# Kernel optimization log

Measured on AMD Instinct MI355X. Metric: run time of the kernel, lower is better.

The kernel has to match this reference:

```python
import jax, jax.numpy as jnp
import numpy as np

B, S, D, H = 2, 2048, 1024, 16
DK = D // H
THETA = 10000.0


def apply_rope(x, pos, theta):
    # x: [B, H, S, DK], pos: [S]
    dk = x.shape[-1]
    inv_freq = 1.0 / (theta ** (jnp.arange(0, dk, 2, dtype=jnp.float32) / dk))  # [DK/2]
    ang = pos.astype(jnp.float32)[:, None] * inv_freq[None, :]  # [S, DK/2]
    cos, sin = jnp.cos(ang), jnp.sin(ang)
    x1 = x[..., 0::2]  # even dims
    x2 = x[..., 1::2]  # odd dims
    r1 = x1 * cos - x2 * sin
    r2 = x1 * sin + x2 * cos
    # re-interleave pairs back into last dim
    return jnp.stack([r1, r2], axis=-1).reshape(x.shape)


def setup_inputs() -> dict:
    key = jax.random.key(0)
    k1, k2, k3 = jax.random.split(key, 3)
    in_features = jax.random.normal(k1, (B, S, D), dtype=jnp.float32)
    token_positions = jnp.arange(S, dtype=jnp.int32)
    Wqkv = jax.random.normal(k2, (D, 3 * D), dtype=jnp.float32) * 0.02
    Wo = jax.random.normal(k3, (D, D), dtype=jnp.float32) * 0.02
    return {"in_features": in_features, "token_positions": token_positions,
            "Wqkv": Wqkv, "Wo": Wo}


def reference(in_features, token_positions, Wqkv, Wo):
    x = in_features
    qkv = x @ Wqkv  # [B, S, 3D]
    Q, K, V = jnp.split(qkv, 3, axis=-1)

    def to_heads(t):  # [B, S, D] -> [B, H, S, DK]
        return t.reshape(B, S, H, DK).transpose(0, 2, 1, 3)

    Q, K, V = to_heads(Q), to_heads(K), to_heads(V)
    Q = apply_rope(Q, token_positions, THETA)
    K = apply_rope(K, token_positions, THETA)

    scale = 1.0 / jnp.sqrt(jnp.float32(DK))
    scores = jnp.einsum("bhqd,bhkd->bhqk", Q, K) * scale  # [B, H, S, S]
    causal = jnp.tril(jnp.ones((S, S), dtype=bool))
    scores = jnp.where(causal, scores, jnp.finfo(scores.dtype).min)
    attn = jax.nn.softmax(scores, axis=-1)
    out = jnp.einsum("bhqk,bhkd->bhqd", attn, V)  # [B, H, S, DK]
    out = out.transpose(0, 2, 1, 3).reshape(B, S, D)
    return out @ Wo
```

## Files before the change

### kernel.cpp

```cpp
#include <hip/hip_runtime.h>
#include <hip/hip_bf16.h>
#include <math.h>

typedef unsigned short u16;
typedef unsigned int u32;
typedef __attribute__((ext_vector_type(4))) float f32x4;
typedef __attribute__((ext_vector_type(8))) short bf16x8;

#define B_ 2
#define S_ 2048
#define D_ 1024
#define H_ 16
#define DK_ 64

__device__ __forceinline__ float exp2_fast(float x) {
    return __builtin_amdgcn_exp2f(x);
}

__device__ __forceinline__ u16 f2bf(float x) {
    union { __hip_bfloat16 h; u16 u; } v;
    v.h = __float2bfloat16(x);
    return v.u;
}

__device__ __forceinline__ u32 cvt_pk_bf16(float a, float b) {
    u32 r;
    asm("v_cvt_pk_bf16_f32 %0, %1, %2" : "=v"(r) : "v"(a), "v"(b));
    return r;
}

__device__ __forceinline__ void gload_lds16(const u16* g, u16* l) {
    __builtin_amdgcn_global_load_lds(
        (const __attribute__((address_space(1))) unsigned int*)g,
        (__attribute__((address_space(3))) unsigned int*)l, 16, 0, 0);
}

__global__ __launch_bounds__(256) void cast_bf16_kernel(
    const float* __restrict__ in, u16* __restrict__ outp, int n)
{
    const int i = (blockIdx.x * 256 + threadIdx.x) * 8;
    if (i >= n) return;
    float4 a = *(const float4*)(in + i);
    float4 b = *(const float4*)(in + i + 4);
    u32 p0 = (u32)f2bf(a.x) | ((u32)f2bf(a.y) << 16);
    u32 p1 = (u32)f2bf(a.z) | ((u32)f2bf(a.w) << 16);
    u32 p2 = (u32)f2bf(b.x) | ((u32)f2bf(b.y) << 16);
    u32 p3 = (u32)f2bf(b.z) | ((u32)f2bf(b.w) << 16);
    *(uint4*)(outp + i) = make_uint4(p0, p1, p2, p3);
}

__global__ __launch_bounds__(256) void transpose_cast(
    const float* __restrict__ W, u16* __restrict__ WT, int N)
{
    __shared__ float tile[64][65];
    const int k0 = blockIdx.x * 64, n0 = blockIdx.y * 64;
    const int t = threadIdx.x;
    const int r = t >> 4, c4 = (t & 15) * 4;
#pragma unroll
    for (int p = 0; p < 4; ++p) {
        float4 v = *(const float4*)&W[(size_t)(k0 + r + p * 16) * N + n0 + c4];
        tile[r + p * 16][c4 + 0] = v.x;
        tile[r + p * 16][c4 + 1] = v.y;
        tile[r + p * 16][c4 + 2] = v.z;
        tile[r + p * 16][c4 + 3] = v.w;
    }
    __syncthreads();
    const int nl = t >> 2, kc = (t & 3) * 16;
    u16 buf[16];
#pragma unroll
    for (int j = 0; j < 16; ++j) buf[j] = f2bf(tile[kc + j][nl]);
    const size_t idx = (size_t)(n0 + nl) * 1024 + k0 + kc;
    u32 px[8];
#pragma unroll
    for (int j = 0; j < 8; ++j) px[j] = (u32)buf[2 * j] | ((u32)buf[2 * j + 1] << 16);
    *(uint4*)&WT[idx]     = make_uint4(px[0], px[1], px[2], px[3]);
    *(uint4*)&WT[idx + 8] = make_uint4(px[4], px[5], px[6], px[7]);
}

__global__ __launch_bounds__(256) void rope_table_kernel(
    const int* __restrict__ pos, float2* __restrict__ tab)
{
    const int i = blockIdx.x * 256 + threadIdx.x;
    const int s = i >> 5, j = i & 31;
    const float freq = __powf(10000.f, -(float)(2 * j) * (1.f / 64.f));
    const float ang = (float)pos[s] * freq;
    float sn, cs;
    sincosf(ang, &sn, &cs);
    tab[i] = make_float2(cs, sn);
}

__device__ __forceinline__ void gemm_mainloop_128x64(
    const u16* __restrict__ A, const u16* __restrict__ BT, int K,
    int m0, int n0, int tid, int l, int w,
    u16* lA, u16* lB, f32x4 acc[2][4])
{
    const int wr = w >> 1, wc = w & 1, lr = l & 15, lg = l >> 4;
    const int srow = tid >> 3;
    const int cg   = (tid & 7) ^ (srow & 7);
    const u16* gA = A + (size_t)(m0 + srow) * K + cg * 8;
    const u16* gB = BT + (size_t)(n0 + srow) * K + cg * 8;
    const int dst0 = tid * 8;

#define GSTAGE(k0, off)                                              \
    do {                                                             \
        gload_lds16(gA + (k0),          lA + (off) + dst0);          \
        gload_lds16(gA + (k0) + 64 * K, lA + (off) + 4096 + dst0);   \
        gload_lds16(gB + (k0),          lB + (off) + dst0);          \
        gload_lds16(gB + (k0) + 64 * K, lB + (off) + 4096 + dst0);   \
    } while (0)

    GSTAGE(0, 0);

    const int NT = K >> 6;
    for (int t = 0; t < NT; ++t) {
        const int coff = (t & 1) * 8192;
        if (t + 1 < NT) {
            GSTAGE((t + 1) * 64, coff ^ 8192);
            asm volatile("s_waitcnt vmcnt(4)" ::: "memory");
        } else {
            asm volatile("s_waitcnt vmcnt(0)" ::: "memory");
        }
        __builtin_amdgcn_s_barrier();
        __builtin_amdgcn_sched_barrier(0);

        bf16x8 a[2][2], b[4][2];
#pragma unroll
        for (int i = 0; i < 2; ++i) {
            const int row = wr * 32 + i * 16 + lr;
#pragma unroll
            for (int s = 0; s < 2; ++s)
                a[i][s] = *(const bf16x8*)(lA + coff + row * 64 + (((s * 4 + lg) ^ (row & 7)) * 8));
        }
#pragma unroll
        for (int j = 0; j < 4; ++j) {
            const int row = wc * 64 + j * 16 + lr;
#pragma unroll
            for (int s = 0; s < 2; ++s)
                b[j][s] = *(const bf16x8*)(lB + coff + row * 64 + (((s * 4 + lg) ^ (row & 7)) * 8));
        }
#pragma unroll
        for (int s = 0; s < 2; ++s)
#pragma unroll
            for (int i = 0; i < 2; ++i)
#pragma unroll
                for (int j = 0; j < 4; ++j)
                    acc[i][j] = __builtin_amdgcn_mfma_f32_16x16x32_bf16(a[i][s], b[j][s], acc[i][j], 0, 0, 0);

        asm volatile("s_waitcnt lgkmcnt(0)" ::: "memory");
        __builtin_amdgcn_s_barrier();
        __builtin_amdgcn_sched_barrier(0);
    }
#undef GSTAGE
}

__global__ __launch_bounds__(512, 4) void gemm_qkv_rope(
    const u16* __restrict__ A, const u16* __restrict__ BT,
    const float2* __restrict__ tab,
    u16* __restrict__ qo, u16* __restrict__ ko, u16* __restrict__ vto)
{
    __shared__ u16 lA[2 * 128 * 64];
    __shared__ u16 lB[2 * 128 * 64];
    const int tid = threadIdx.x, l = tid & 63, w = tid >> 6;
    const int m0 = blockIdx.x * 128, n0 = blockIdx.y * 128;

    f32x4 acc[2][4] = {};
    gemm_mainloop_128x64(A, BT, 1024, m0, n0, tid, l, w, lA, lB, acc);

    const int wr = w >> 1, wc = w & 1, lr = l & 15, lg = l >> 4;
    const int region = n0 >> 10;

    if (region < 2) {
        u16* dst = (region == 0) ? qo : ko;
        const float qscale = (region == 0) ? (0.125f * 1.44269504088896f) : 1.0f;
#pragma unroll
        for (int j = 0; j < 4; ++j) {
            const int nb = n0 + wc * 64 + j * 16;
            const int h = (nb >> 6) & 15;
            const int c = j * 16 + lr;
#pragma unroll
            for (int i = 0; i < 2; ++i) {
#pragma unroll
                for (int r = 0; r < 4; ++r) {
                    const int m = m0 + wr * 32 + i * 16 + lg * 4 + r;
                    const int bb = m >> 11, s = m & (S_ - 1);
                    const float2 cs = tab[s * 32 + (c >> 1)];
                    const float v = acc[i][j][r];
                    const float vp = __shfl_xor(v, 1);
                    float outv = ((lr & 1) == 0) ? (v * cs.x - vp * cs.y)
                                                 : (v * cs.x + vp * cs.y);
                    outv *= qscale;
                    dst[(((size_t)bb * H_ + h) * S_ + s) * DK_ + c] = f2bf(outv);
                }
            }
        }
    } else {
#pragma unroll
        for (int j = 0; j < 4; ++j) {
            const int nb = n0 + wc * 64 + j * 16;
            const int h = (nb >> 6) & 15;
            const int c = j * 16 + lr;
#pragma unroll
            for (int i = 0; i < 2; ++i) {
#pragma unroll
                for (int r = 0; r < 4; ++r) {
                    const int m = m0 + wr * 32 + i * 16 + lg * 4 + r;
                    const int bb = m >> 11, s = m & (S_ - 1);
                    vto[(((size_t)bb * H_ + h) * DK_ + c) * S_ + s] = f2bf(acc[i][j][r]);
                }
            }
        }
    }
}

__device__ __forceinline__ void stage_tile(
    const u16* __restrict__ Kbh, const u16* __restrict__ Vbh, int kt,
    u16* sKb, u16* sVb, int w, int sr0, int cg)
{
    gload_lds16(Kbh + ((size_t)kt * 64 + sr0) * DK_ + cg * 8,     sKb + w * 1024);
    gload_lds16(Kbh + ((size_t)kt * 64 + sr0 + 8) * DK_ + cg * 8, sKb + w * 1024 + 512);
    gload_lds16(Vbh + (size_t)sr0 * S_ + kt * 64 + cg * 8,        sVb + w * 1024);
    gload_lds16(Vbh + (size_t)(sr0 + 8) * S_ + kt * 64 + cg * 8,  sVb + w * 1024 + 512);
}

__device__ __forceinline__ void attn_stripe(
    int qt, int bh, int w, int l, int lr, int lg,
    const u16* __restrict__ Qg, const u16* __restrict__ Kg,
    const u16* __restrict__ VTg, u16* __restrict__ Og,
    u16 (*sK)[64 * 64], u16 (*sV)[64 * 64])
{
    const int q0 = qt * 64 + w * 16;
    const u16* Kbh = Kg + (size_t)bh * S_ * DK_;
    const u16* Vbh = VTg + (size_t)bh * DK_ * S_;

    const u16* Qp = Qg + ((size_t)bh * S_ + q0) * DK_;
    bf16x8 qa[2];
    qa[0] = *(const bf16x8*)(Qp + lr * DK_ + lg * 8);
    qa[1] = *(const bf16x8*)(Qp + lr * DK_ + 32 + lg * 8);

    const int sr0 = w * 16 + (l >> 3);
    const int cg  = (l & 7) ^ (sr0 & 7);

    f32x4 o[4] = {};
    float mi = -3.0e38f, li = 0.f;

    const int s0 = lr + 32 * (lg & 1);
    const int s1 = s0 + 16;
    const bool hi2 = (lg >= 2);

    stage_tile(Kbh, Vbh, 0, sK[0], sV[0], w, sr0, cg);
    asm volatile("s_waitcnt vmcnt(0)" ::: "memory");
    __syncthreads();

    for (int kt = 0; kt <= qt; ++kt) {
        const int cur = kt & 1;
        if (kt < qt)
            stage_tile(Kbh, Vbh, kt + 1, sK[cur ^ 1], sV[cur ^ 1], w, sr0, cg);

        f32x4 s4[4] = {};
        __builtin_amdgcn_s_setprio(1);
#pragma unroll
        for (int kf = 0; kf < 4; ++kf) {
            const int row = kf * 16 + lr;
#pragma unroll
            for (int ks = 0; ks < 2; ++ks) {
                bf16x8 kb = *(const bf16x8*)(&sK[cur][row * 64 + (((ks * 4 + lg) ^ (row & 7)) * 8)]);
                s4[kf] = __builtin_amdgcn_mfma_f32_16x16x32_bf16(kb, qa[ks], s4[kf], 0, 0, 0);
            }
        }
        __builtin_amdgcn_s_setprio(0);
        if (kt == qt) {
            const int qloc = w * 16 + lr;
#pragma unroll
            for (int kf = 0; kf < 4; ++kf)
#pragma unroll
                for (int r = 0; r < 4; ++r)
                    if (kf * 16 + lg * 4 + r > qloc) s4[kf][r] = -3.0e38f;
        }

        float mx = s4[0][0];
#pragma unroll
        for (int kf = 0; kf < 4; ++kf)
#pragma unroll
            for (int r = 0; r < 4; ++r) mx = fmaxf(mx, s4[kf][r]);
        mx = fmaxf(mx, __shfl_xor(mx, 16));
        mx = fmaxf(mx, __shfl_xor(mx, 32));
        if (mx > mi + 8.0f) {
            const float al = exp2_fast(mi - mx);
            mi = mx;
            li *= al;
#pragma unroll
            for (int jf = 0; jf < 4; ++jf)
#pragma unroll
                for (int r = 0; r < 4; ++r) o[jf][r] *= al;
        }
        float rs = 0.f;
#pragma unroll
        for (int kf = 0; kf < 4; ++kf)
#pragma unroll
            for (int r = 0; r < 4; ++r) {
                const float p = exp2_fast(s4[kf][r] - mi);
                s4[kf][r] = p;
                rs += p;
            }
        rs += __shfl_xor(rs, 16);
        rs += __shfl_xor(rs, 32);
        li += rs;

        u32 pk[4][2];
#pragma unroll
        for (int kf = 0; kf < 4; ++kf) {
            pk[kf][0] = cvt_pk_bf16(s4[kf][0], s4[kf][1]);
            pk[kf][1] = cvt_pk_bf16(s4[kf][2], s4[kf][3]);
        }
        union { u32 wd[4]; bf16x8 v; } pa[2];
#pragma unroll
        for (int ks = 0; ks < 2; ++ks) {
            const u32 lo0 = pk[2 * ks][0],     lo1 = pk[2 * ks][1];
            const u32 hi0 = pk[2 * ks + 1][0], hi1 = pk[2 * ks + 1][1];
            const u32 a0 = __shfl(lo0, s0), b0 = __shfl(hi0, s0);
            const u32 a1 = __shfl(lo1, s0), b1 = __shfl(hi1, s0);
            const u32 a2 = __shfl(lo0, s1), b2 = __shfl(hi0, s1);
            const u32 a3 = __shfl(lo1, s1), b3 = __shfl(hi1, s1);
            pa[ks].wd[0] = hi2 ? b0 : a0;
            pa[ks].wd[1] = hi2 ? b1 : a1;
            pa[ks].wd[2] = hi2 ? b2 : a2;
            pa[ks].wd[3] = hi2 ? b3 : a3;
        }

        __builtin_amdgcn_s_setprio(1);
#pragma unroll
        for (int ks = 0; ks < 2; ++ks) {
#pragma unroll
            for (int jf = 0; jf < 4; ++jf) {
                const int row = jf * 16 + lr;
                bf16x8 vb = *(const bf16x8*)(&sV[cur][row * 64 + (((ks * 4 + lg) ^ (row & 7)) * 8)]);
                o[jf] = __builtin_amdgcn_mfma_f32_16x16x32_bf16(vb, pa[ks].v, o[jf], 0, 0, 0);
            }
        }
        __builtin_amdgcn_s_setprio(0);

        asm volatile("s_waitcnt vmcnt(0)" ::: "memory");
        __syncthreads();
    }

    const float inv = 1.f / li;
    const int b = bh >> 4, h = bh & 15;
    const int srow = q0 + lr;
    u16* orow = Og + ((size_t)b * S_ + srow) * D_ + h * DK_;
#pragma unroll
    for (int jf = 0; jf < 4; ++jf) {
#pragma unroll
        for (int p = 0; p < 2; ++p) {
            const u32 wv = cvt_pk_bf16(o[jf][2 * p] * inv, o[jf][2 * p + 1] * inv);
            *(u32*)(orow + jf * 16 + lg * 4 + 2 * p) = wv;
        }
    }
}

__global__ __launch_bounds__(256) void attn_mfma(
    const u16* __restrict__ Qg, const u16* __restrict__ Kg,
    const u16* __restrict__ VTg, u16* __restrict__ Og)
{
    __shared__ u16 sK[2][64 * 64];
    __shared__ u16 sV[2][64 * 64];
    const int t = threadIdx.x, l = t & 63, w = t >> 6;
    const int lr = l & 15, lg = l >> 4;
    const int bh = blockIdx.x;
    const int qt = 31 - blockIdx.y;
    attn_stripe(qt, bh, w, l, lr, lg, Qg, Kg, VTg, Og, sK, sV);
}

__global__ __launch_bounds__(512, 4) void gemm_out(
    const u16* __restrict__ A, const u16* __restrict__ BT, float* __restrict__ C)
{
    __shared__ u16 lA[2 * 128 * 64];
    __shared__ u16 lB[2 * 128 * 64];
    const int tid = threadIdx.x, l = tid & 63, w = tid >> 6;
    const int m0 = blockIdx.x * 128, n0 = blockIdx.y * 128;

    f32x4 acc[2][4] = {};
    gemm_mainloop_128x64(A, BT, 1024, m0, n0, tid, l, w, lA, lB, acc);

    const int wr = w >> 1, wc = w & 1, lr = l & 15, lg = l >> 4;
#pragma unroll
    for (int j = 0; j < 4; ++j) {
        const int n = n0 + wc * 64 + j * 16 + lr;
#pragma unroll
        for (int i = 0; i < 2; ++i) {
#pragma unroll
            for (int r = 0; r < 4; ++r) {
                const int m = m0 + wr * 32 + i * 16 + lg * 4 + r;
                C[(size_t)m * D_ + n] = acc[i][j][r];
            }
        }
    }
}

extern "C" void kernel_launch(void* const* d_in, const int* in_sizes, int n_in,
                              void* d_out, int out_size, void* d_ws, size_t ws_size,
                              hipStream_t stream) {
    const float* X    = (const float*)d_in[0];
    const int*   pos  = (const int*)d_in[1];
    const float* Wqkv = (const float*)d_in[2];
    const float* Wo   = (const float*)d_in[3];
    float* out = (float*)d_out;

    char* ws = (char*)d_ws;
    u16*    Xb  = (u16*)(ws);
    u16*    WqT = (u16*)(ws + ((size_t)8  << 20));
    u16*    WoT = (u16*)(ws + ((size_t)14 << 20));
    float2* tab = (float2*)(ws + ((size_t)16 << 20));
    u16*    Qb  = (u16*)(ws + ((size_t)17 << 20));
    u16*    Kb  = (u16*)(ws + ((size_t)25 << 20));
    u16*    VTb = (u16*)(ws + ((size_t)33 << 20));
    u16*    AOb = (u16*)(ws + ((size_t)41 << 20));

    cast_bf16_kernel<<<2048, 256, 0, stream>>>(X, Xb, B_ * S_ * D_);
    transpose_cast<<<dim3(16, 48), 256, 0, stream>>>(Wqkv, WqT, 3 * D_);
    transpose_cast<<<dim3(16, 16), 256, 0, stream>>>(Wo, WoT, D_);
    rope_table_kernel<<<256, 256, 0, stream>>>(pos, tab);

    gemm_qkv_rope<<<dim3(32, 24), 512, 0, stream>>>(Xb, WqT, tab, Qb, Kb, VTb);
    attn_mfma<<<dim3(32, 32), 256, 0, stream>>>(Qb, Kb, VTb, AOb);
    gemm_out<<<dim3(32, 8), 512, 0, stream>>>(AOb, WoT, out);
}
```

Measured before the change: 119.9 us.

## Widen attention KV tile from 64 to 128 keys per iteration

The attention kernel now stages 128-key K/V tiles per loop iteration instead of 64, halving the number of iterations, barriers and softmax rescale steps. The LDS layout changes to 128-wide V rows with a 16-way XOR swizzle, and the causal mask now covers the diagonal 128-block using the query's position inside it. In exchange, LDS use doubles, register pressure rises with s4[8] and pa[4], and for odd query tiles half of the last key tile is computed and then masked, which is wasted work.

```diff
diff --git a/kernel.cpp b/kernel.cpp
--- a/kernel.cpp
+++ b/kernel.cpp
@@ -212,23 +212,21 @@
     }
 }
 
-__device__ __forceinline__ void stage_tile(
-    const u16* __restrict__ Kbh, const u16* __restrict__ Vbh, int kt,
-    u16* sKb, u16* sVb, int w, int sr0, int cg)
-{
-    gload_lds16(Kbh + ((size_t)kt * 64 + sr0) * DK_ + cg * 8,     sKb + w * 1024);
-    gload_lds16(Kbh + ((size_t)kt * 64 + sr0 + 8) * DK_ + cg * 8, sKb + w * 1024 + 512);
-    gload_lds16(Vbh + (size_t)sr0 * S_ + kt * 64 + cg * 8,        sVb + w * 1024);
-    gload_lds16(Vbh + (size_t)(sr0 + 8) * S_ + kt * 64 + cg * 8,  sVb + w * 1024 + 512);
-}
-
-__device__ __forceinline__ void attn_stripe(
-    int qt, int bh, int w, int l, int lr, int lg,
+__global__ __launch_bounds__(256) void attn_mfma(
     const u16* __restrict__ Qg, const u16* __restrict__ Kg,
-    const u16* __restrict__ VTg, u16* __restrict__ Og,
-    u16 (*sK)[64 * 64], u16 (*sV)[64 * 64])
-{
+    const u16* __restrict__ VTg, u16* __restrict__ Og)
+{
+    __shared__ u16 sK[2][128 * 64];
+    __shared__ u16 sV[2][64 * 128];
+    const int t = threadIdx.x, l = t & 63, w = t >> 6;
+    const int lr = l & 15, lg = l >> 4;
+    const int bh = blockIdx.x;
+    const int qt = 31 - blockIdx.y;
     const int q0 = qt * 64 + w * 16;
+    const int dt = qt >> 1;
+    const int NT = dt + 1;
+    const int qloc = (qt & 1) * 64 + w * 16 + lr;
+
     const u16* Kbh = Kg + (size_t)bh * S_ * DK_;
     const u16* Vbh = VTg + (size_t)bh * DK_ * S_;
 
@@ -237,8 +235,24 @@
     qa[0] = *(const bf16x8*)(Qp + lr * DK_ + lg * 8);
     qa[1] = *(const bf16x8*)(Qp + lr * DK_ + 32 + lg * 8);
 
-    const int sr0 = w * 16 + (l >> 3);
-    const int cg  = (l & 7) ^ (sr0 & 7);
+    const int kcg = (l & 7) ^ (l >> 3);
+
+#define STAGE(kt, b)                                                          \
+    do {                                                                      \
+        _Pragma("unroll")                                                     \
+        for (int i = 0; i < 4; ++i) {                                         \
+            const int kr = w * 32 + i * 8 + (l >> 3);                         \
+            gload_lds16(Kbh + ((size_t)(kt) * 128 + kr) * DK_ + kcg * 8,      \
+                        &sK[b][(w * 32 + i * 8) * 64]);                       \
+        }                                                                     \
+        _Pragma("unroll")                                                     \
+        for (int i = 0; i < 4; ++i) {                                         \
+            const int vr = w * 16 + i * 4 + (l >> 4);                         \
+            const int vc = (l & 15) ^ ((i * 4 + (l >> 4)) & 15);              \
+            gload_lds16(Vbh + (size_t)vr * S_ + (kt) * 128 + vc * 8,          \
+                        &sV[b][(w * 16 + i * 4) * 128]);                      \
+        }                                                                     \
+    } while (0)
 
     f32x4 o[4] = {};
     float mi = -3.0e38f, li = 0.f;
@@ -247,19 +261,18 @@
     const int s1 = s0 + 16;
     const bool hi2 = (lg >= 2);
 
-    stage_tile(Kbh, Vbh, 0, sK[0], sV[0], w, sr0, cg);
+    STAGE(0, 0);
     asm volatile("s_waitcnt vmcnt(0)" ::: "memory");
     __syncthreads();
 
-    for (int kt = 0; kt <= qt; ++kt) {
+    for (int kt = 0; kt < NT; ++kt) {
         const int cur = kt & 1;
-        if (kt < qt)
-            stage_tile(Kbh, Vbh, kt + 1, sK[cur ^ 1], sV[cur ^ 1], w, sr0, cg);
-
-        f32x4 s4[4] = {};
+        if (kt + 1 < NT) STAGE(kt + 1, cur ^ 1);
+
+        f32x4 s4[8] = {};
         __builtin_amdgcn_s_setprio(1);
 #pragma unroll
-        for (int kf = 0; kf < 4; ++kf) {
+        for (int kf = 0; kf < 8; ++kf) {
             const int row = kf * 16 + lr;
 #pragma unroll
             for (int ks = 0; ks < 2; ++ks) {
@@ -268,10 +281,9 @@
             }
         }
         __builtin_amdgcn_s_setprio(0);
-        if (kt == qt) {
-            const int qloc = w * 16 + lr;
-#pragma unroll
-            for (int kf = 0; kf < 4; ++kf)
+        if (kt == dt) {
+#pragma unroll
+            for (int kf = 0; kf < 8; ++kf)
 #pragma unroll
                 for (int r = 0; r < 4; ++r)
                     if (kf * 16 + lg * 4 + r > qloc) s4[kf][r] = -3.0e38f;
@@ -279,7 +291,7 @@
 
         float mx = s4[0][0];
 #pragma unroll
-        for (int kf = 0; kf < 4; ++kf)
+        for (int kf = 0; kf < 8; ++kf)
 #pragma unroll
             for (int r = 0; r < 4; ++r) mx = fmaxf(mx, s4[kf][r]);
         mx = fmaxf(mx, __shfl_xor(mx, 16));
@@ -295,7 +307,7 @@
         }
         float rs = 0.f;
 #pragma unroll
-        for (int kf = 0; kf < 4; ++kf)
+        for (int kf = 0; kf < 8; ++kf)
 #pragma unroll
             for (int r = 0; r < 4; ++r) {
                 const float p = exp2_fast(s4[kf][r] - mi);
@@ -306,15 +318,15 @@
         rs += __shfl_xor(rs, 32);
         li += rs;
 
-        u32 pk[4][2];
-#pragma unroll
-        for (int kf = 0; kf < 4; ++kf) {
+        u32 pk[8][2];
+#pragma unroll
+        for (int kf = 0; kf < 8; ++kf) {
             pk[kf][0] = cvt_pk_bf16(s4[kf][0], s4[kf][1]);
             pk[kf][1] = cvt_pk_bf16(s4[kf][2], s4[kf][3]);
         }
-        union { u32 wd[4]; bf16x8 v; } pa[2];
-#pragma unroll
-        for (int ks = 0; ks < 2; ++ks) {
+        union { u32 wd[4]; bf16x8 v; } pa[4];
+#pragma unroll
+        for (int ks = 0; ks < 4; ++ks) {
             const u32 lo0 = pk[2 * ks][0],     lo1 = pk[2 * ks][1];
             const u32 hi0 = pk[2 * ks + 1][0], hi1 = pk[2 * ks + 1][1];
             const u32 a0 = __shfl(lo0, s0), b0 = __shfl(hi0, s0);
@@ -329,11 +341,11 @@
 
         __builtin_amdgcn_s_setprio(1);
 #pragma unroll
-        for (int ks = 0; ks < 2; ++ks) {
+        for (int ks = 0; ks < 4; ++ks) {
 #pragma unroll
             for (int jf = 0; jf < 4; ++jf) {
                 const int row = jf * 16 + lr;
-                bf16x8 vb = *(const bf16x8*)(&sV[cur][row * 64 + (((ks * 4 + lg) ^ (row & 7)) * 8)]);
+                bf16x8 vb = *(const bf16x8*)(&sV[cur][row * 128 + (((ks * 4 + lg) ^ (row & 15)) * 8)]);
                 o[jf] = __builtin_amdgcn_mfma_f32_16x16x32_bf16(vb, pa[ks].v, o[jf], 0, 0, 0);
             }
         }
@@ -342,6 +354,7 @@
         asm volatile("s_waitcnt vmcnt(0)" ::: "memory");
         __syncthreads();
     }
+#undef STAGE
 
     const float inv = 1.f / li;
     const int b = bh >> 4, h = bh & 15;
@@ -355,19 +368,6 @@
             *(u32*)(orow + jf * 16 + lg * 4 + 2 * p) = wv;
         }
     }
-}
-
-__global__ __launch_bounds__(256) void attn_mfma(
-    const u16* __restrict__ Qg, const u16* __restrict__ Kg,
-    const u16* __restrict__ VTg, u16* __restrict__ Og)
-{
-    __shared__ u16 sK[2][64 * 64];
-    __shared__ u16 sV[2][64 * 64];
-    const int t = threadIdx.x, l = t & 63, w = t >> 6;
-    const int lr = l & 15, lg = l >> 4;
-    const int bh = blockIdx.x;
-    const int qt = 31 - blockIdx.y;
-    attn_stripe(qt, bh, w, l, lr, lg, Qg, Kg, VTg, Og, sK, sV);
 }
 
 __global__ __launch_bounds__(512, 4) void gemm_out(
```

Measured after the change: 114.2 us. 4.8% less time.

## Triple-buffer K in LDS with depth-2 prefetch; load V straight into registers

Applied to the files above, without the earlier changes.

The attention kernel now stages only K tiles through LDS, using three buffers and prefetching two tiles ahead. V fragments are loaded directly from global memory into registers at the start of each iteration, so the QK MFMAs and softmax hide their latency. The end-of-iteration wait drops from vmcnt(0) to lgkmcnt(0) plus a raw barrier, and launch bounds now request 4 blocks per CU thanks to the smaller LDS footprint. The max and sum reductions are also rewritten as balanced trees. The risks are that K readiness now depends implicitly on the compiler's vmcnt waits for the V loads, and that uncached V reads from global may stall the PV MFMAs.

```diff
diff --git a/kernel.cpp b/kernel.cpp
--- a/kernel.cpp
+++ b/kernel.cpp
@@ -212,23 +212,18 @@
     }
 }
 
-__device__ __forceinline__ void stage_tile(
-    const u16* __restrict__ Kbh, const u16* __restrict__ Vbh, int kt,
-    u16* sKb, u16* sVb, int w, int sr0, int cg)
-{
-    gload_lds16(Kbh + ((size_t)kt * 64 + sr0) * DK_ + cg * 8,     sKb + w * 1024);
-    gload_lds16(Kbh + ((size_t)kt * 64 + sr0 + 8) * DK_ + cg * 8, sKb + w * 1024 + 512);
-    gload_lds16(Vbh + (size_t)sr0 * S_ + kt * 64 + cg * 8,        sVb + w * 1024);
-    gload_lds16(Vbh + (size_t)(sr0 + 8) * S_ + kt * 64 + cg * 8,  sVb + w * 1024 + 512);
-}
-
-__device__ __forceinline__ void attn_stripe(
-    int qt, int bh, int w, int l, int lr, int lg,
+__global__ __launch_bounds__(256, 4) void attn_mfma(
     const u16* __restrict__ Qg, const u16* __restrict__ Kg,
-    const u16* __restrict__ VTg, u16* __restrict__ Og,
-    u16 (*sK)[64 * 64], u16 (*sV)[64 * 64])
-{
+    const u16* __restrict__ VTg, u16* __restrict__ Og)
+{
+    __shared__ u16 sK[3][64 * 64];
+    const int t = threadIdx.x, l = t & 63, w = t >> 6;
+    const int lr = l & 15, lg = l >> 4;
+    const int bh = blockIdx.x;
+    const int qt = 31 - blockIdx.y;
     const int q0 = qt * 64 + w * 16;
+    const int NT = qt + 1;
+
     const u16* Kbh = Kg + (size_t)bh * S_ * DK_;
     const u16* Vbh = VTg + (size_t)bh * DK_ * S_;
 
@@ -240,6 +235,14 @@
     const int sr0 = w * 16 + (l >> 3);
     const int cg  = (l & 7) ^ (sr0 & 7);
 
+#define STAGE_K(kt, b)                                                        \
+    do {                                                                      \
+        gload_lds16(Kbh + ((size_t)(kt) * 64 + sr0) * DK_ + cg * 8,           \
+                    &sK[b][w * 1024]);                                        \
+        gload_lds16(Kbh + ((size_t)(kt) * 64 + sr0 + 8) * DK_ + cg * 8,       \
+                    &sK[b][w * 1024 + 512]);                                  \
+    } while (0)
+
     f32x4 o[4] = {};
     float mi = -3.0e38f, li = 0.f;
 
@@ -247,14 +250,28 @@
     const int s1 = s0 + 16;
     const bool hi2 = (lg >= 2);
 
-    stage_tile(Kbh, Vbh, 0, sK[0], sV[0], w, sr0, cg);
-    asm volatile("s_waitcnt vmcnt(0)" ::: "memory");
-    __syncthreads();
-
-    for (int kt = 0; kt <= qt; ++kt) {
-        const int cur = kt & 1;
-        if (kt < qt)
-            stage_tile(Kbh, Vbh, kt + 1, sK[cur ^ 1], sV[cur ^ 1], w, sr0, cg);
+    STAGE_K(0, 0);
+    if (NT > 1) {
+        STAGE_K(1, 1);
+        asm volatile("s_waitcnt vmcnt(2)" ::: "memory");
+    } else {
+        asm volatile("s_waitcnt vmcnt(0)" ::: "memory");
+    }
+    __builtin_amdgcn_s_barrier();
+    __builtin_amdgcn_sched_barrier(0);
+
+    int cur = 0;
+    for (int kt = 0; kt < NT; ++kt) {
+        bf16x8 vb[4][2];
+#pragma unroll
+        for (int jf = 0; jf < 4; ++jf)
+#pragma unroll
+            for (int ks = 0; ks < 2; ++ks)
+                vb[jf][ks] = *(const bf16x8*)(Vbh + (size_t)(jf * 16 + lr) * S_
+                                              + kt * 64 + ks * 32 + lg * 8);
+
+        const int nb = (cur == 0) ? 2 : cur - 1;
+        if (kt + 2 < NT) STAGE_K(kt + 2, nb);
 
         f32x4 s4[4] = {};
         __builtin_amdgcn_s_setprio(1);
@@ -277,11 +294,11 @@
                     if (kf * 16 + lg * 4 + r > qloc) s4[kf][r] = -3.0e38f;
         }
 
-        float mx = s4[0][0];
+        float m4[4];
 #pragma unroll
         for (int kf = 0; kf < 4; ++kf)
-#pragma unroll
-            for (int r = 0; r < 4; ++r) mx = fmaxf(mx, s4[kf][r]);
+            m4[kf] = fmaxf(fmaxf(s4[kf][0], s4[kf][1]), fmaxf(s4[kf][2], s4[kf][3]));
+        float mx = fmaxf(fmaxf(m4[0], m4[1]), fmaxf(m4[2], m4[3]));
         mx = fmaxf(mx, __shfl_xor(mx, 16));
         mx = fmaxf(mx, __shfl_xor(mx, 32));
         if (mx > mi + 8.0f) {
@@ -293,15 +310,14 @@
 #pragma unroll
                 for (int r = 0; r < 4; ++r) o[jf][r] *= al;
         }
-        float rs = 0.f;
-#pragma unroll
-        for (int kf = 0; kf < 4; ++kf)
-#pragma unroll
-            for (int r = 0; r < 4; ++r) {
-                const float p = exp2_fast(s4[kf][r] - mi);
-                s4[kf][r] = p;
-                rs += p;
-            }
+        float r4[4];
+#pragma unroll
+        for (int kf = 0; kf < 4; ++kf) {
+#pragma unroll
+            for (int r = 0; r < 4; ++r) s4[kf][r] = exp2_fast(s4[kf][r] - mi);
+            r4[kf] = (s4[kf][0] + s4[kf][1]) + (s4[kf][2] + s4[kf][3]);
+        }
+        float rs = (r4[0] + r4[1]) + (r4[2] + r4[3]);
         rs += __shfl_xor(rs, 16);
         rs += __shfl_xor(rs, 32);
         li += rs;
@@ -329,19 +345,18 @@
 
         __builtin_amdgcn_s_setprio(1);
 #pragma unroll
-        for (int ks = 0; ks < 2; ++ks) {
-#pragma unroll
-            for (int jf = 0; jf < 4; ++jf) {
-                const int row = jf * 16 + lr;
-                bf16x8 vb = *(const bf16x8*)(&sV[cur][row * 64 + (((ks * 4 + lg) ^ (row & 7)) * 8)]);
-                o[jf] = __builtin_amdgcn_mfma_f32_16x16x32_bf16(vb, pa[ks].v, o[jf], 0, 0, 0);
-            }
-        }
+        for (int ks = 0; ks < 2; ++ks)
+#pragma unroll
+            for (int jf = 0; jf < 4; ++jf)
+                o[jf] = __builtin_amdgcn_mfma_f32_16x16x32_bf16(vb[jf][ks], pa[ks].v, o[jf], 0, 0, 0);
         __builtin_amdgcn_s_setprio(0);
 
-        asm volatile("s_waitcnt vmcnt(0)" ::: "memory");
-        __syncthreads();
-    }
+        asm volatile("s_waitcnt lgkmcnt(0)" ::: "memory");
+        __builtin_amdgcn_s_barrier();
+        __builtin_amdgcn_sched_barrier(0);
+        cur = (cur == 2) ? 0 : cur + 1;
+    }
+#undef STAGE_K
 
     const float inv = 1.f / li;
     const int b = bh >> 4, h = bh & 15;
@@ -355,19 +370,6 @@
             *(u32*)(orow + jf * 16 + lg * 4 + 2 * p) = wv;
         }
     }
-}
-
-__global__ __launch_bounds__(256) void attn_mfma(
-    const u16* __restrict__ Qg, const u16* __restrict__ Kg,
-    const u16* __restrict__ VTg, u16* __restrict__ Og)
-{
-    __shared__ u16 sK[2][64 * 64];
-    __shared__ u16 sV[2][64 * 64];
-    const int t = threadIdx.x, l = t & 63, w = t >> 6;
-    const int lr = l & 15, lg = l >> 4;
-    const int bh = blockIdx.x;
-    const int qt = 31 - blockIdx.y;
-    attn_stripe(qt, bh, w, l, lr, lg, Qg, Kg, VTg, Og, sK, sV);
 }
 
 __global__ __launch_bounds__(512, 4) void gemm_out(
```

New measurement: 155.8 us. 1.3x slower.
